# Performance work log

Measured on AMD Instinct MI355X. Metric: run time of the kernel, lower is better.

Reference implementation:

```python
import jax, jax.numpy as jnp
import numpy as np
from jax.scipy.special import logsumexp

EPS = 0.1
NUM_ITERS = 50
TOPO_MULT = 1.0


def _dist_cosine(x):
    # x: [N, D] -> pairwise cosine distance [N, N], clamped to >= 0
    norms = jnp.sqrt(jnp.clip(jnp.sum(x * x, axis=1, keepdims=True), 1e-8, None))
    xn = x / norms
    return jnp.clip(1.0 - xn @ xn.T, 0.0, None)


def _sinkhorn_log_domain(a, b, C):
    # a, b: [N, N] row-stochastic; C: [N, N]. Duals computed with no grad (detached).
    log_a = jnp.log(jnp.clip(a, 1e-8, None))
    log_b = jnp.log(jnp.clip(b, 1e-8, None))
    la = jax.lax.stop_gradient(log_a)
    lb = jax.lax.stop_gradient(log_b)
    lC = jax.lax.stop_gradient(-C / EPS)[None]  # [1, N, N]

    def body(i, fg):
        f, g = fg
        g = EPS * lb - EPS * logsumexp(f[:, :, None] + lC, axis=1)
        f = EPS * la - EPS * logsumexp(lC + g[:, None, :], axis=2)
        return (f, g)

    f0 = jnp.zeros_like(a)
    f, g = jax.lax.fori_loop(0, NUM_ITERS, body, (f0, f0))
    cost = jnp.sum(a * f, axis=1) + jnp.sum(b * g, axis=1)  # [N]
    return jnp.mean(cost)


def reference(x_original, x_reconstructed, z_latent, log_sigma_lat, log_var_recon, log_var_topo):
    recon_loss = jnp.mean((x_reconstructed - x_original) ** 2)

    D_orig = _dist_cosine(x_original)   # [N, N]
    D_latent = _dist_cosine(z_latent)   # [N, N]

    sigma_orig = jnp.median(D_orig)
    sigma_orig = jnp.where(sigma_orig == 0, jnp.asarray(1e-6, D_orig.dtype), sigma_orig)
    sigma_lat = jax.nn.softplus(log_sigma_lat) + 1e-6  # [1]

    S_orig = jnp.exp(-D_orig ** 2 / (2.0 * sigma_orig ** 2))
    S_lat = jnp.exp(-D_latent ** 2 / (2.0 * sigma_lat ** 2))

    N = S_orig.shape[0]
    mask = 1.0 - jnp.eye(N, dtype=S_orig.dtype)
    S_orig = S_orig * mask
    S_lat = S_lat * mask

    P_orig = S_orig / jnp.clip(jnp.sum(S_orig, axis=1, keepdims=True), 1e-8, None)
    P_lat = S_lat / jnp.clip(jnp.sum(S_lat, axis=1, keepdims=True), 1e-8, None)

    C = D_orig
    ot_orig_lat = _sinkhorn_log_domain(P_orig, P_lat, C)
    ot_lat_lat = _sinkhorn_log_domain(P_lat, P_lat, C)
    ot_orig_orig = _sinkhorn_log_domain(P_orig, P_orig, C)

    topo_loss = jnp.clip(ot_orig_lat - 0.5 * ot_lat_lat - 0.5 * ot_orig_orig, 0.0, None)
    topo_loss = topo_loss * TOPO_MULT

    prec_r = jnp.exp(-log_var_recon)  # [1]
    prec_t = jnp.exp(-log_var_topo)   # [1]
    total_loss = (0.5 * prec_r * recon_loss + 0.5 * log_var_recon
                  + 0.5 * prec_t * topo_loss + 0.5 * log_var_topo)  # [1]
    return (total_loss, recon_loss, topo_loss)


def setup_inputs() -> dict:
    key = jax.random.key(0)
    k1, k2, k3 = jax.random.split(key, 3)
    N, D, DL = 256, 4096, 256
    return {
        "x_original": jax.random.normal(k1, (N, D), dtype=jnp.float32),
        "x_reconstructed": jax.random.normal(k2, (N, D), dtype=jnp.float32),
        "z_latent": jax.random.normal(k3, (N, DL), dtype=jnp.float32),
        "log_sigma_lat": jnp.zeros((1,), dtype=jnp.float32),
        "log_var_recon": jnp.zeros((1,), dtype=jnp.float32),
        "log_var_topo": jnp.zeros((1,), dtype=jnp.float32),
    }
```

## Files before the change

### kernel.cpp

```cpp
#include <hip/hip_runtime.h>
#include <hip/hip_fp16.h>

#define EPS 0.1f
#define SINK_ITERS 50
#define KSCALE_LN 9.0109133472f
#define USTRIDE 272

typedef _Float16 f16;
typedef _Float16 f16x4 __attribute__((ext_vector_type(4)));
typedef _Float16 f16x8 __attribute__((ext_vector_type(8)));
typedef float f32x4 __attribute__((ext_vector_type(4)));

#define PIN_U4(v) asm volatile("" : "+v"(v.x), "+v"(v.y), "+v"(v.z), "+v"(v.w))

__device__ __forceinline__ float wave_red_sum(float v) {
    #pragma unroll
    for (int o = 32; o; o >>= 1) v += __shfl_xor(v, o, 64);
    return v;
}

__global__ __launch_bounds__(256) void k_pre(const float4* __restrict__ xo,
                                             const float4* __restrict__ xr,
                                             const float4* __restrict__ z,
                                             f16x4* __restrict__ xh,
                                             f16x4* __restrict__ zh,
                                             float* __restrict__ acc) {
    __shared__ float red[4];
    int b = blockIdx.x, t = threadIdx.x;
    if (b < 512) {
        int tid = b * 256 + t;
        float s = 0.f;
        for (int i = tid; i < 262144; i += 512 * 256) {
            float4 a = xo[i], r = xr[i];
            float d0 = r.x - a.x, d1 = r.y - a.y, d2 = r.z - a.z, d3 = r.w - a.w;
            s = fmaf(d0, d0, s); s = fmaf(d1, d1, s);
            s = fmaf(d2, d2, s); s = fmaf(d3, d3, s);
        }
        s = wave_red_sum(s);
        if ((t & 63) == 0) red[t >> 6] = s;
        __syncthreads();
        if (t == 0) atomicAdd(acc + 3, red[0] + red[1] + red[2] + red[3]);
    } else {
        int row = b - 512;
        const float4* src; f16x4* dst; int c4;
        if (row < 256) { src = xo + (size_t)row * 1024; dst = xh + (size_t)row * 1024; c4 = 1024; }
        else { src = z + (size_t)(row - 256) * 64; dst = zh + (size_t)(row - 256) * 64; c4 = 64; }
        float s = 0.f;
        for (int i = t; i < c4; i += 256) {
            float4 v = src[i];
            s = fmaf(v.x, v.x, s); s = fmaf(v.y, v.y, s);
            s = fmaf(v.z, v.z, s); s = fmaf(v.w, v.w, s);
        }
        s = wave_red_sum(s);
        if ((t & 63) == 0) red[t >> 6] = s;
        __syncthreads();
        float tot = red[0] + red[1] + red[2] + red[3];
        float rn = 1.f / sqrtf(fmaxf(tot, 1e-8f));
        for (int i = t; i < c4; i += 256) {
            float4 v = src[i];
            f16x4 h;
            h[0] = (f16)(v.x * rn); h[1] = (f16)(v.y * rn);
            h[2] = (f16)(v.z * rn); h[3] = (f16)(v.w * rn);
            dst[i] = h;
        }
    }
}

__global__ __launch_bounds__(256) void k_gemm_f16(const uint4* __restrict__ xh,
                                                  const uint4* __restrict__ zh,
                                                  float* __restrict__ part,
                                                  float* __restrict__ part2) {
    __shared__ __align__(16) f16 Ai[64 * 40], Bj[64 * 40];
    int zb = blockIdx.z;
    const uint4* X; int lda8, k0, nchunk; float* out;
    if (zb < 16) { X = xh; lda8 = 512; k0 = zb * 256; nchunk = 8; out = part + (size_t)zb * 65536; }
    else { X = zh; lda8 = 32; k0 = (zb - 16) * 64; nchunk = 2; out = part2 + (size_t)(zb - 16) * 65536; }
    int i0 = blockIdx.x * 64, j0 = blockIdx.y * 64;
    int t = threadIdx.x, lane = t & 63, wv = t >> 6;
    int m16 = lane & 15, quad = lane >> 4;
    int r = t >> 2, ko = (t & 3) * 8;
    f32x4 acc[4] = {};
    for (int ch = 0; ch < nchunk; ch++) {
        int kb8 = (k0 + ch * 32) >> 3;
        uint4 va = X[(size_t)(i0 + r) * lda8 + kb8 + (t & 3)];
        uint4 vb = X[(size_t)(j0 + r) * lda8 + kb8 + (t & 3)];
        __syncthreads();
        *(uint4*)&Ai[r * 40 + ko] = va;
        *(uint4*)&Bj[r * 40 + ko] = vb;
        __syncthreads();
        f16x8 a = *(const f16x8*)&Ai[(wv * 16 + m16) * 40 + quad * 8];
        #pragma unroll
        for (int st = 0; st < 4; st++) {
            f16x8 bfr = *(const f16x8*)&Bj[(st * 16 + m16) * 40 + quad * 8];
            acc[st] = __builtin_amdgcn_mfma_f32_16x16x32_f16(a, bfr, acc[st], 0, 0, 0);
        }
    }
    #pragma unroll
    for (int st = 0; st < 4; st++)
        #pragma unroll
        for (int reg = 0; reg < 4; reg++)
            out[(i0 + wv * 16 + quad * 4 + reg) * 256 + j0 + st * 16 + m16] = acc[st][reg];
}

__global__ __launch_bounds__(256) void k_reduce_do(const float* __restrict__ part,
                                                   float* __restrict__ Do) {
    int e = blockIdx.x * 256 + threadIdx.x;
    float s = 0.f;
    for (int sl = 0; sl < 16; sl++) s += part[(size_t)sl * 65536 + e];
    Do[e] = fmaxf(1.f - s, 0.f);
}

__device__ __forceinline__ int med_bin(float v) {
    int b = (int)(v * 4096.f);
    if (v < (float)b * (1.f / 4096.f)) b--;
    else if (v >= (float)(b + 1) * (1.f / 4096.f)) b++;
    if (b < 0) b = 0;
    if (b > 8191) b = 8191;
    return b;
}

__global__ __launch_bounds__(1024) void k_median(const float* __restrict__ D,
                                                 float* __restrict__ out_sigma) {
    __shared__ int hist[8192];
    __shared__ int redc[16];
    __shared__ int sh_bin[2];
    __shared__ int sh_tot;
    int t = threadIdx.x;
    unsigned r[64];
    #pragma unroll
    for (int i = 0; i < 64; i++) r[i] = __float_as_uint(D[t + i * 1024]);
    #pragma unroll
    for (int j = 0; j < 8; j++) hist[t + j * 1024] = 0;
    __syncthreads();
    #pragma unroll
    for (int i = 0; i < 64; i++)
        atomicAdd(&hist[med_bin(__uint_as_float(r[i]))], 1);
    __syncthreads();
    int s8 = 0;
    #pragma unroll
    for (int j = 0; j < 8; j++) s8 += hist[t * 8 + j];
    int inc = s8;
    #pragma unroll
    for (int o = 1; o < 64; o <<= 1) {
        int vv = __shfl_up(inc, o, 64);
        if ((t & 63) >= o) inc += vv;
    }
    if ((t & 63) == 63) redc[t >> 6] = inc;
    __syncthreads();
    int woff = 0;
    for (int wv = 0; wv < (t >> 6); wv++) woff += redc[wv];
    int excl = woff + inc - s8;
    for (int sel = 0; sel < 2; sel++) {
        int k = 32767 + sel;
        if (excl <= k && k < excl + s8) {
            int cum = excl, bfound = 8191;
            bool found = false;
            for (int j = 0; j < 8; j++) {
                int hc = hist[t * 8 + j];
                if (!found) {
                    if (cum + hc > k) { bfound = t * 8 + j; found = true; }
                    else cum += hc;
                }
            }
            sh_bin[sel] = bfound;
        }
    }
    __syncthreads();
    unsigned res[2];
    for (int sel = 0; sel < 2; sel++) {
        int k = 32767 + sel;
        int b = sh_bin[sel];
        unsigned lo = __float_as_uint((float)b * (1.f / 4096.f));
        unsigned hi = __float_as_uint((float)(b + 1) * (1.f / 4096.f));
        while (hi - lo > 1u) {
            unsigned mid = (lo + hi) >> 1;
            int c = 0;
            #pragma unroll
            for (int i = 0; i < 64; i++) c += (r[i] < mid) ? 1 : 0;
            #pragma unroll
            for (int o = 32; o; o >>= 1) c += __shfl_xor(c, o, 64);
            if ((t & 63) == 0) redc[t >> 6] = c;
            __syncthreads();
            if (t == 0) {
                int tot = 0;
                for (int wv = 0; wv < 16; wv++) tot += redc[wv];
                sh_tot = tot;
            }
            __syncthreads();
            if (sh_tot <= k) lo = mid; else hi = mid;
        }
        res[sel] = lo;
    }
    if (t == 0)
        out_sigma[0] = 0.5f * (__uint_as_float(res[0]) + __uint_as_float(res[1]));
}

__global__ __launch_bounds__(256) void k_prep(const float* __restrict__ Do,
                                              const float* __restrict__ part2,
                                              const float* __restrict__ wsacc,
                                              const float* __restrict__ lsl,
                                              float* __restrict__ Po, float* __restrict__ Pl,
                                              float* __restrict__ ELo, float* __restrict__ ELl,
                                              f16* __restrict__ Kh) {
    __shared__ float red[8];
    int i = blockIdx.x, j = threadIdx.x;
    int e = i * 256 + j;
    float sig_o = wsacc[4];
    if (sig_o == 0.f) sig_o = 1e-6f;
    float x = lsl[0];
    float sp = (x > 20.f) ? x : log1pf(__expf(x));
    float sig_l = sp + 1e-6f;
    float i2o = 1.f / (2.f * sig_o * sig_o);
    float i2l = 1.f / (2.f * sig_l * sig_l);
    float d_o = Do[e];
    float sD = part2[e] + part2[65536 + e] + part2[131072 + e] + part2[196608 + e];
    float d_l = fmaxf(1.f - sD, 0.f);
    float so = (i == j) ? 0.f : __expf(-d_o * d_o * i2o);
    float sl = (i == j) ? 0.f : __expf(-d_l * d_l * i2l);
    float wso = wave_red_sum(so);
    float wsl = wave_red_sum(sl);
    if ((j & 63) == 0) { red[j >> 6] = wso; red[4 + (j >> 6)] = wsl; }
    __syncthreads();
    float sum_o = red[0] + red[1] + red[2] + red[3];
    float sum_l = red[4] + red[5] + red[6] + red[7];
    float po = so / fmaxf(sum_o, 1e-8f);
    float pl = sl / fmaxf(sum_l, 1e-8f);
    Po[e] = po;
    Pl[e] = pl;
    ELo[e] = EPS * __logf(fmaxf(po, 1e-8f));
    ELl[e] = EPS * __logf(fmaxf(pl, 1e-8f));
    float kv = __expf(-d_o * (1.f / EPS) + KSCALE_LN);
    Kh[(((i >> 3) * 256 + j) << 3) + (i & 7)] = (f16)kv;
}

__global__ __launch_bounds__(512, 2) void k_sinkhorn(const float* __restrict__ Po,
                                                     const float* __restrict__ Pl,
                                                     const float* __restrict__ ELo,
                                                     const float* __restrict__ ELl,
                                                     const uint4* __restrict__ Kq,
                                                     float* __restrict__ wsacc) {
    __shared__ __align__(16) f16 U[2][4 * USTRIDE];
    __shared__ float CW[8][4];
    int t = threadIdx.x;
    int lane = t & 63, wv = t >> 6;
    int m16 = lane & 15, quad = lane >> 4;
    int w = blockIdx.x;
    int s = w >> 6;
    int ibase = (w & 63) * 4;

    uint4 bf0[8], bf1[8];
    int cA = 32 * wv + m16, cB = cA + 16;
    #pragma unroll
    for (int kc = 0; kc < 8; kc++) {
        bf0[kc] = Kq[(kc * 4 + quad) * 256 + cA];
        bf1[kc] = Kq[(kc * 4 + quad) * 256 + cB];
    }
    #pragma unroll
    for (int kc = 0; kc < 8; kc++) { PIN_U4(bf0[kc]); PIN_U4(bf1[kc]); }

    const float* ELa_b = (s == 1 ? ELl : ELo);
    const float* ELb_b = (s == 2 ? ELo : ELl);
    float ela[2][4] = {}, elb[2][4] = {};
    if (quad == 0) {
        #pragma unroll
        for (int reg = 0; reg < 4; reg++) {
            int i = ibase + reg;
            ela[0][reg] = ELa_b[i * 256 + cA] + EPS * KSCALE_LN;
            ela[1][reg] = ELa_b[i * 256 + cB] + EPS * KSCALE_LN;
            elb[0][reg] = ELb_b[i * 256 + cA] + EPS * KSCALE_LN;
            elb[1][reg] = ELb_b[i * 256 + cB] + EPS * KSCALE_LN;
        }
    }

    if (t < 136)
        *(uint4*)&U[0][t * 8] =
            make_uint4(0x3C003C00u, 0x3C003C00u, 0x3C003C00u, 0x3C003C00u);
    __syncthreads();

    float df[2][4] = {}, dg[2][4] = {};
    for (int it = 0; it < 2 * SINK_ITERS; it++) {
        const f16* ub = &U[it & 1][0];
        f16* un = &U[(it + 1) & 1][0];
        f32x4 acc0 = {0.f, 0.f, 0.f, 0.f}, acc1 = {0.f, 0.f, 0.f, 0.f};
        #pragma unroll
        for (int kc = 0; kc < 8; kc++) {
            f16x8 a = *(const f16x8*)&ub[(m16 & 3) * USTRIDE + kc * 32 + quad * 8];
            acc0 = __builtin_amdgcn_mfma_f32_16x16x32_f16(a, __builtin_bit_cast(f16x8, bf0[kc]),
                                                          acc0, 0, 0, 0);
            acc1 = __builtin_amdgcn_mfma_f32_16x16x32_f16(a, __builtin_bit_cast(f16x8, bf1[kc]),
                                                          acc1, 0, 0, 0);
        }
        bool fstep = (it & 1);
        if (quad == 0) {
            #pragma unroll
            for (int reg = 0; reg < 4; reg++) {
                float z0 = acc0[reg], z1 = acc1[reg];
                float e0 = fstep ? ela[0][reg] : elb[0][reg];
                float e1 = fstep ? ela[1][reg] : elb[1][reg];
                float d0 = e0 - EPS * __logf(z0);
                float d1 = e1 - EPS * __logf(z1);
                if (fstep) { df[0][reg] = d0; df[1][reg] = d1; }
                else       { dg[0][reg] = d0; dg[1][reg] = d1; }
                un[reg * USTRIDE + cA] = (f16)__expf(d0);
                un[reg * USTRIDE + cB] = (f16)__expf(d1);
            }
        }
        __syncthreads();
    }

    const float* PaB = (s == 1 ? Pl : Po);
    const float* PbB = (s == 2 ? Po : Pl);
    float cs[4] = {};
    if (quad == 0) {
        #pragma unroll
        for (int reg = 0; reg < 4; reg++) {
            int i = ibase + reg;
            cs[reg] = PaB[i * 256 + cA] * df[0][reg] + PbB[i * 256 + cA] * dg[0][reg] +
                      PaB[i * 256 + cB] * df[1][reg] + PbB[i * 256 + cB] * dg[1][reg];
        }
    }
    #pragma unroll
    for (int o = 1; o < 16; o <<= 1) {
        #pragma unroll
        for (int reg = 0; reg < 4; reg++) cs[reg] += __shfl_xor(cs[reg], o, 64);
    }
    if (lane == 0) {
        #pragma unroll
        for (int reg = 0; reg < 4; reg++) CW[wv][reg] = cs[reg];
    }
    __syncthreads();
    if (t == 0) {
        float v = 0.f;
        for (int w2 = 0; w2 < 8; w2++)
            v += CW[w2][0] + CW[w2][1] + CW[w2][2] + CW[w2][3];
        atomicAdd(&wsacc[s], v);
    }
}

__global__ void k_final(const float* __restrict__ wsacc, const float* __restrict__ lvr_p,
                        const float* __restrict__ lvt_p, float* __restrict__ out) {
    float recon = wsacc[3] * (1.f / (256.f * 4096.f));
    float ot0 = wsacc[0] * (1.f / 256.f);
    float ot1 = wsacc[1] * (1.f / 256.f);
    float ot2 = wsacc[2] * (1.f / 256.f);
    float topo = ot0 - 0.5f * ot1 - 0.5f * ot2;
    topo = topo > 0.f ? topo : 0.f;
    float lvr = lvr_p[0], lvt = lvt_p[0];
    out[0] = 0.5f * __expf(-lvr) * recon + 0.5f * lvr +
             0.5f * __expf(-lvt) * topo + 0.5f * lvt;
    out[1] = recon;
    out[2] = topo;
}

extern "C" void kernel_launch(void* const* d_in, const int* in_sizes, int n_in,
                              void* d_out, int out_size, void* d_ws, size_t ws_size,
                              hipStream_t stream) {
    const float* xo = (const float*)d_in[0];
    const float* xr = (const float*)d_in[1];
    const float* z  = (const float*)d_in[2];
    const float* lsl = (const float*)d_in[3];
    const float* lvr = (const float*)d_in[4];
    const float* lvt = (const float*)d_in[5];
    float* out = (float*)d_out;
    float* ws = (float*)d_ws;

    float* acc = ws;
    float* xh  = ws + 64;
    float* zh  = xh + 524288;
    float* Do  = zh + 32768;
    float* Po  = Do + 65536;
    float* Pl  = Po + 65536;
    float* ELo = Pl + 65536;
    float* ELl = ELo + 65536;
    float* Kh  = ELl + 65536;
    float* part = Kh + 32768;
    float* part2 = Po;

    hipMemsetAsync(acc, 0, 64, stream);
    k_pre<<<1024, 256, 0, stream>>>((const float4*)xo, (const float4*)xr, (const float4*)z,
                                    (f16x4*)xh, (f16x4*)zh, acc);
    k_gemm_f16<<<dim3(4, 4, 20), 256, 0, stream>>>((const uint4*)xh, (const uint4*)zh,
                                                   part, part2);
    k_reduce_do<<<256, 256, 0, stream>>>(part, Do);
    k_median<<<1, 1024, 0, stream>>>(Do, acc + 4);
    k_prep<<<256, 256, 0, stream>>>(Do, part2, acc, lsl, Po, Pl, ELo, ELl, (f16*)Kh);
    k_sinkhorn<<<192, 512, 0, stream>>>(Po, Pl, ELo, ELl, (const uint4*)Kh, acc);
    k_final<<<1, 1, 0, stream>>>(acc, lvr, lvt, out);
}
```

Measured before the change: 223.2 us.

## Halve Sinkhorn block to 4 waves with 64 columns each and all-lane epilogue

The Sinkhorn kernel now runs 256 threads per block instead of 512. Each wave holds four 16-column K tiles in registers and splits the K reduction across two accumulator sets, which gives more independent MFMA chains. All 64 lanes now do the log/exp update by picking their column's result with a select, instead of only quad 0. The dual values are precomputed in exponentiated form, and the final potentials are rebuilt only from the last two iterations' sums. The cost is higher register pressure, with 128 VGPRs pinned for K, and fewer waves to hide barrier latency.

Result: faster. 206.3 us (-7.6%).

```diff
diff --git a/kernel.cpp b/kernel.cpp
--- a/kernel.cpp
+++ b/kernel.cpp
@@ -17,6 +17,12 @@
     #pragma unroll
     for (int o = 32; o; o >>= 1) v += __shfl_xor(v, o, 64);
     return v;
+}
+
+__device__ __forceinline__ float sel4(int q, float a, float b, float c, float d) {
+    float ab = (q & 1) ? b : a;
+    float cd = (q & 1) ? d : c;
+    return (q & 2) ? cd : ab;
 }
 
 __global__ __launch_bounds__(256) void k_pre(const float4* __restrict__ xo,
@@ -233,43 +239,44 @@
     Kh[(((i >> 3) * 256 + j) << 3) + (i & 7)] = (f16)kv;
 }
 
-__global__ __launch_bounds__(512, 2) void k_sinkhorn(const float* __restrict__ Po,
+__global__ __launch_bounds__(256, 1) void k_sinkhorn(const float* __restrict__ Po,
                                                      const float* __restrict__ Pl,
                                                      const float* __restrict__ ELo,
                                                      const float* __restrict__ ELl,
                                                      const uint4* __restrict__ Kq,
                                                      float* __restrict__ wsacc) {
     __shared__ __align__(16) f16 U[2][4 * USTRIDE];
-    __shared__ float CW[8][4];
+    __shared__ float CW[4][4];
     int t = threadIdx.x;
     int lane = t & 63, wv = t >> 6;
     int m16 = lane & 15, quad = lane >> 4;
     int w = blockIdx.x;
     int s = w >> 6;
     int ibase = (w & 63) * 4;
-
-    uint4 bf0[8], bf1[8];
-    int cA = 32 * wv + m16, cB = cA + 16;
-    #pragma unroll
-    for (int kc = 0; kc < 8; kc++) {
-        bf0[kc] = Kq[(kc * 4 + quad) * 256 + cA];
-        bf1[kc] = Kq[(kc * 4 + quad) * 256 + cB];
-    }
-    #pragma unroll
-    for (int kc = 0; kc < 8; kc++) { PIN_U4(bf0[kc]); PIN_U4(bf1[kc]); }
+    int colbase = wv * 64;
+    int c_lane = colbase + quad * 16 + m16;
+
+    uint4 bf[4][8];
+    #pragma unroll
+    for (int ct = 0; ct < 4; ct++)
+        #pragma unroll
+        for (int kc = 0; kc < 8; kc++)
+            bf[ct][kc] = Kq[(kc * 4 + quad) * 256 + colbase + ct * 16 + m16];
+    #pragma unroll
+    for (int ct = 0; ct < 4; ct++)
+        #pragma unroll
+        for (int kc = 0; kc < 8; kc++) PIN_U4(bf[ct][kc]);
 
     const float* ELa_b = (s == 1 ? ELl : ELo);
     const float* ELb_b = (s == 2 ? ELo : ELl);
-    float ela[2][4] = {}, elb[2][4] = {};
-    if (quad == 0) {
-        #pragma unroll
-        for (int reg = 0; reg < 4; reg++) {
-            int i = ibase + reg;
-            ela[0][reg] = ELa_b[i * 256 + cA] + EPS * KSCALE_LN;
-            ela[1][reg] = ELa_b[i * 256 + cB] + EPS * KSCALE_LN;
-            elb[0][reg] = ELb_b[i * 256 + cA] + EPS * KSCALE_LN;
-            elb[1][reg] = ELb_b[i * 256 + cB] + EPS * KSCALE_LN;
-        }
+    float ef[4], eg[4], Ef[4], Eg[4];
+    #pragma unroll
+    for (int reg = 0; reg < 4; reg++) {
+        int i = ibase + reg;
+        ef[reg] = ELa_b[i * 256 + c_lane] + EPS * KSCALE_LN;
+        eg[reg] = ELb_b[i * 256 + c_lane] + EPS * KSCALE_LN;
+        Ef[reg] = __expf(ef[reg]);
+        Eg[reg] = __expf(eg[reg]);
     }
 
     if (t < 136)
@@ -277,53 +284,65 @@
             make_uint4(0x3C003C00u, 0x3C003C00u, 0x3C003C00u, 0x3C003C00u);
     __syncthreads();
 
-    float df[2][4] = {}, dg[2][4] = {};
+    float zf[4], zg[4];
     for (int it = 0; it < 2 * SINK_ITERS; it++) {
         const f16* ub = &U[it & 1][0];
         f16* un = &U[(it + 1) & 1][0];
-        f32x4 acc0 = {0.f, 0.f, 0.f, 0.f}, acc1 = {0.f, 0.f, 0.f, 0.f};
-        #pragma unroll
-        for (int kc = 0; kc < 8; kc++) {
-            f16x8 a = *(const f16x8*)&ub[(m16 & 3) * USTRIDE + kc * 32 + quad * 8];
-            acc0 = __builtin_amdgcn_mfma_f32_16x16x32_f16(a, __builtin_bit_cast(f16x8, bf0[kc]),
-                                                          acc0, 0, 0, 0);
-            acc1 = __builtin_amdgcn_mfma_f32_16x16x32_f16(a, __builtin_bit_cast(f16x8, bf1[kc]),
-                                                          acc1, 0, 0, 0);
+        f16x8 a[8];
+        #pragma unroll
+        for (int kc = 0; kc < 8; kc++)
+            a[kc] = *(const f16x8*)&ub[(m16 & 3) * USTRIDE + kc * 32 + quad * 8];
+        f32x4 accA[4] = {{0.f,0.f,0.f,0.f},{0.f,0.f,0.f,0.f},{0.f,0.f,0.f,0.f},{0.f,0.f,0.f,0.f}};
+        f32x4 accB[4] = {{0.f,0.f,0.f,0.f},{0.f,0.f,0.f,0.f},{0.f,0.f,0.f,0.f},{0.f,0.f,0.f,0.f}};
+        #pragma unroll
+        for (int kc = 0; kc < 4; kc++)
+            #pragma unroll
+            for (int ct = 0; ct < 4; ct++)
+                accA[ct] = __builtin_amdgcn_mfma_f32_16x16x32_f16(
+                    a[kc], __builtin_bit_cast(f16x8, bf[ct][kc]), accA[ct], 0, 0, 0);
+        #pragma unroll
+        for (int kc = 4; kc < 8; kc++)
+            #pragma unroll
+            for (int ct = 0; ct < 4; ct++)
+                accB[ct] = __builtin_amdgcn_mfma_f32_16x16x32_f16(
+                    a[kc], __builtin_bit_cast(f16x8, bf[ct][kc]), accB[ct], 0, 0, 0);
+        float zsum[4];
+        #pragma unroll
+        for (int reg = 0; reg < 4; reg++) {
+            float zA = sel4(quad, accA[0][reg], accA[1][reg], accA[2][reg], accA[3][reg]);
+            float zB = sel4(quad, accB[0][reg], accB[1][reg], accB[2][reg], accB[3][reg]);
+            zsum[reg] = zA + zB;
+        }
+        if (it == 2 * SINK_ITERS - 2) {
+            #pragma unroll
+            for (int reg = 0; reg < 4; reg++) zg[reg] = zsum[reg];
+        }
+        if (it == 2 * SINK_ITERS - 1) {
+            #pragma unroll
+            for (int reg = 0; reg < 4; reg++) zf[reg] = zsum[reg];
         }
         bool fstep = (it & 1);
-        if (quad == 0) {
-            #pragma unroll
-            for (int reg = 0; reg < 4; reg++) {
-                float z0 = acc0[reg], z1 = acc1[reg];
-                float e0 = fstep ? ela[0][reg] : elb[0][reg];
-                float e1 = fstep ? ela[1][reg] : elb[1][reg];
-                float d0 = e0 - EPS * __logf(z0);
-                float d1 = e1 - EPS * __logf(z1);
-                if (fstep) { df[0][reg] = d0; df[1][reg] = d1; }
-                else       { dg[0][reg] = d0; dg[1][reg] = d1; }
-                un[reg * USTRIDE + cA] = (f16)__expf(d0);
-                un[reg * USTRIDE + cB] = (f16)__expf(d1);
-            }
+        #pragma unroll
+        for (int reg = 0; reg < 4; reg++) {
+            float E = fstep ? Ef[reg] : Eg[reg];
+            float p = __expf(-EPS * __logf(zsum[reg]));
+            un[reg * USTRIDE + c_lane] = (f16)(E * p);
         }
         __syncthreads();
     }
 
     const float* PaB = (s == 1 ? Pl : Po);
     const float* PbB = (s == 2 ? Po : Pl);
-    float cs[4] = {};
-    if (quad == 0) {
-        #pragma unroll
-        for (int reg = 0; reg < 4; reg++) {
-            int i = ibase + reg;
-            cs[reg] = PaB[i * 256 + cA] * df[0][reg] + PbB[i * 256 + cA] * dg[0][reg] +
-                      PaB[i * 256 + cB] * df[1][reg] + PbB[i * 256 + cB] * dg[1][reg];
-        }
-    }
-    #pragma unroll
-    for (int o = 1; o < 16; o <<= 1) {
-        #pragma unroll
-        for (int reg = 0; reg < 4; reg++) cs[reg] += __shfl_xor(cs[reg], o, 64);
-    }
+    float cs[4];
+    #pragma unroll
+    for (int reg = 0; reg < 4; reg++) {
+        int i = ibase + reg;
+        float dfv = ef[reg] - EPS * __logf(zf[reg]);
+        float dgv = eg[reg] - EPS * __logf(zg[reg]);
+        cs[reg] = PaB[i * 256 + c_lane] * dfv + PbB[i * 256 + c_lane] * dgv;
+    }
+    #pragma unroll
+    for (int reg = 0; reg < 4; reg++) cs[reg] = wave_red_sum(cs[reg]);
     if (lane == 0) {
         #pragma unroll
         for (int reg = 0; reg < 4; reg++) CW[wv][reg] = cs[reg];
@@ -331,7 +350,7 @@
     __syncthreads();
     if (t == 0) {
         float v = 0.f;
-        for (int w2 = 0; w2 < 8; w2++)
+        for (int w2 = 0; w2 < 4; w2++)
             v += CW[w2][0] + CW[w2][1] + CW[w2][2] + CW[w2][3];
         atomicAdd(&wsacc[s], v);
     }
@@ -376,7 +395,7 @@
     float* part = Kh + 32768;
     float* part2 = Po;
 
-    hipMemsetAsync(acc, 0, 64, stream);
+    (void)hipMemsetAsync(acc, 0, 64, stream);
     k_pre<<<1024, 256, 0, stream>>>((const float4*)xo, (const float4*)xr, (const float4*)z,
                                     (f16x4*)xh, (f16x4*)zh, acc);
     k_gemm_f16<<<dim3(4, 4, 20), 256, 0, stream>>>((const uint4*)xh, (const uint4*)zh,
@@ -384,6 +403,6 @@
     k_reduce_do<<<256, 256, 0, stream>>>(part, Do);
     k_median<<<1, 1024, 0, stream>>>(Do, acc + 4);
     k_prep<<<256, 256, 0, stream>>>(Do, part2, acc, lsl, Po, Pl, ELo, ELl, (f16*)Kh);
-    k_sinkhorn<<<192, 512, 0, stream>>>(Po, Pl, ELo, ELl, (const uint4*)Kh, acc);
+    k_sinkhorn<<<192, 256, 0, stream>>>(Po, Pl, ELo, ELl, (const uint4*)Kh, acc);
     k_final<<<1, 1, 0, stream>>>(acc, lvr, lvt, out);
 }
```
